# Kernel tuning notes

Measured on AMD Instinct MI355X. Metric: run time of the kernel, lower is better.

Reference implementation:

```python
import jax, jax.numpy as jnp
import numpy as np


def setup_inputs() -> dict:
    key = jax.random.key(0)
    ks = jax.random.split(key, 9)
    B, T, S, D = 4, 256, 256, 512
    scale = 1.0 / np.sqrt(D)
    inp = {
        "output": jax.random.normal(ks[0], (B, T, D), dtype=jnp.float32),
        "context": jax.random.normal(ks[1], (B, S, D), dtype=jnp.float32),
        "mask": jax.random.randint(ks[2], (B, S), 0, 2, dtype=jnp.int32),
        # learned params (nn.Linear stores y = x @ W.T + b; we store W.T directly)
        "Wq": jax.random.normal(ks[3], (D, D), dtype=jnp.float32) * scale,
        "bq": jax.random.normal(ks[4], (D,), dtype=jnp.float32) * scale,
        "Wc": jax.random.normal(ks[5], (D, D), dtype=jnp.float32) * scale,
        "v": jax.random.normal(ks[6], (D,), dtype=jnp.float32) * scale,
        "Wout": jax.random.normal(ks[7], (2 * D, D), dtype=jnp.float32) * scale,
        "bout": jax.random.normal(ks[8], (D,), dtype=jnp.float32) * scale,
    }
    return inp


def reference(output, context, mask, Wq, bq, Wc, v, Wout, bout):
    # output: (B, T, D) decoder states; context: (B, S, D) encoder states
    wq = jnp.einsum("btd,de->bte", output, Wq) + bq          # (B, T, D)
    uh = jnp.einsum("bsd,de->bse", context, Wc)               # (B, S, D)
    # additive score: v . tanh(wq + uh), broadcast over (T, S)
    wquh = jnp.tanh(wq[:, :, None, :] + uh[:, None, :, :])    # (B, T, S, D)
    score = jnp.einsum("btsd,d->bts", wquh, v)                # (B, T, S)
    # masked softmax exactly as the torch code: max over ALL positions,
    # then zero out masked entries (mask==1 means masked) and renormalize.
    max_by_row = jnp.max(score, axis=-1, keepdims=True)
    keep = (1.0 - mask.astype(score.dtype))[:, None, :]       # (B, 1, S)
    attn = jnp.exp(score - max_by_row) * keep
    attn = attn / jnp.sum(attn, axis=-1, keepdims=True)       # (B, T, S)
    mix = jnp.einsum("bts,bsd->btd", attn, context)           # (B, T, D)
    combined = jnp.concatenate([mix, output], axis=-1)        # (B, T, 2D)
    out = jnp.einsum("btf,fd->btd", combined, Wout) + bout    # (B, T, D)
    return out, attn
```

## Files before the change

### kernel.cpp

```cpp
#include <hip/hip_runtime.h>
#include <hip/hip_bf16.h>

#define B_ 4
#define T_ 256
#define S_ 256
#define D_ 512
#define TB 2

typedef __bf16 bf16x8 __attribute__((ext_vector_type(8)));
typedef float  floatx4 __attribute__((ext_vector_type(4)));
typedef float  floatx2 __attribute__((ext_vector_type(2)));

#define C2F 2.885390081777926f

static __device__ __forceinline__ unsigned short f2bf(float x) {
    __hip_bfloat16 h = __float2bfloat16(x);
    return *reinterpret_cast<unsigned short*>(&h);
}
static __device__ __forceinline__ float asf(unsigned int u) {
    float f; __builtin_memcpy(&f, &u, 4); return f;
}
static __device__ __forceinline__ float clamp_pos(float x) {
    return fminf(fmaxf(x, 1e-15f), 1e15f);
}


__global__ __launch_bounds__(256) void prep(
    const float* __restrict__ output, const float* __restrict__ context,
    const float* __restrict__ Wq, const float* __restrict__ Wc,
    const float* __restrict__ Wout,
    unsigned short* __restrict__ out_f, unsigned short* __restrict__ ctx_f,
    unsigned short* __restrict__ Wq_f, unsigned short* __restrict__ Wc_f,
    unsigned short* __restrict__ WoT_f, unsigned short* __restrict__ WoB_f)
{
    const int tid = threadIdx.x;
    const int z = blockIdx.z;

    if (z >= 4) {
        const float* src = (z == 4) ? output : context;
        unsigned short* dst = (z == 4) ? out_f : ctx_f;
        const int bid  = blockIdx.y * 16 + blockIdx.x;
        const int tile = bid * 4 + (tid >> 6);
        const int lane = tid & 63;
        const int mblk = tile >> 4, kblk = tile & 15;
        const float* s = src + (size_t)(mblk * 16 + (lane & 15)) * 512
                             + kblk * 32 + (lane >> 4) * 8;
        float4 a = *(const float4*)s;
        float4 b = *(const float4*)(s + 4);
        uint4 pk;
        pk.x = (unsigned)f2bf(a.x) | ((unsigned)f2bf(a.y) << 16);
        pk.y = (unsigned)f2bf(a.z) | ((unsigned)f2bf(a.w) << 16);
        pk.z = (unsigned)f2bf(b.x) | ((unsigned)f2bf(b.y) << 16);
        pk.w = (unsigned)f2bf(b.z) | ((unsigned)f2bf(b.w) << 16);
        *(uint4*)(dst + (size_t)tile * 512 + lane * 8) = pk;
        return;
    }

    const float* W; unsigned short* WF; int krow0;
    if      (z == 0) { W = Wq;   WF = Wq_f;  krow0 = 0;   }
    else if (z == 1) { W = Wc;   WF = Wc_f;  krow0 = 0;   }
    else if (z == 2) { W = Wout; WF = WoT_f; krow0 = 0;   }
    else             { W = Wout; WF = WoB_f; krow0 = 512; }

    const int n0 = blockIdx.x * 32;
    const int k0 = blockIdx.y * 32;

    __shared__ float tile[32][33];
    const int c = tid & 31, r = tid >> 5;
    #pragma unroll
    for (int i = 0; i < 4; ++i)
        tile[r + 8 * i][c] = W[(size_t)(krow0 + k0 + r + 8 * i) * 512 + n0 + c];
    __syncthreads();
    #pragma unroll
    for (int i = 0; i < 4; ++i) {
        const int n = n0 + r + 8 * i;
        const int k = k0 + c;
        const int tl = (n >> 4) * 16 + (k >> 5);
        const int ln = (n & 15) | (((k >> 3) & 3) << 4);
        WF[((size_t)tl * 64 + ln) * 8 + (k & 7)] = f2bf(tile[c][r + 8 * i]);
    }
}

struct GArgs {
    const unsigned short* Af;
    const unsigned short* Bf;
    const float* aux;
    void* C;
    int mode;
};

__global__ __launch_bounds__(256) void gemm2(GArgs g0, GArgs g1, GArgs g2, GArgs g3)
{
    const int z = blockIdx.z;
    GArgs g = (z == 0) ? g0 : (z == 1) ? g1 : (z == 2) ? g2 : g3;

    const int tid  = threadIdx.x;
    const int wave = tid >> 6, lane = tid & 63;
    const int l15  = lane & 15, quad = lane >> 4;
    const int mblk = blockIdx.y * 4 + wave;
    const int nb0  = blockIdx.x * 4;

    const unsigned short* Ap = g.Af + ((size_t)mblk * 16 * 64 + lane) * 8;
    const unsigned short* Bp = g.Bf + ((size_t)nb0 * 16 * 64 + lane) * 8;

    floatx4 acc[4];
    #pragma unroll
    for (int i = 0; i < 4; ++i) acc[i] = (floatx4){0.f, 0.f, 0.f, 0.f};

    #pragma unroll 4
    for (int k = 0; k < 16; ++k) {
        bf16x8 a  = *(const bf16x8*)(Ap + k * 512);
        #pragma unroll
        for (int ni = 0; ni < 4; ++ni) {
            bf16x8 b = *(const bf16x8*)(Bp + (size_t)ni * 16 * 512 + k * 512);
            acc[ni] = __builtin_amdgcn_mfma_f32_16x16x32_bf16(a, b, acc[ni], 0, 0, 0);
        }
    }

    #pragma unroll
    for (int ni = 0; ni < 4; ++ni) {
        const int col = (nb0 + ni) * 16 + l15;
        const int rbase = mblk * 16 + quad * 4;
        if (g.mode == 1) {
            float* Cf = (float*)g.C;
            float bv = g.aux[col];
            #pragma unroll
            for (int r = 0; r < 4; ++r) {
                float hh = __builtin_amdgcn_exp2f(C2F * (acc[ni][r] + bv));
                Cf[(size_t)(rbase + r) * 512 + col] = clamp_pos(hh);
            }
        } else if (g.mode == 3) {
            unsigned short* Cb = (unsigned short*)g.C;
            float rv = __builtin_amdgcn_rcpf(g.aux[col]);
            rv = fminf(fmaxf(rv, -1e30f), 1e30f);
            #pragma unroll
            for (int r = 0; r < 4; ++r) {
                int row = rbase + r, bb = row >> 8, ss = row & 255;
                float ww = __builtin_amdgcn_exp2f(C2F * acc[ni][r]) * rv;
                ww = fminf(fmaxf(ww, -1e20f), 1e20f);
                Cb[((size_t)(bb * 64 + (col >> 3)) * 256 + ss) * 8 + (col & 7)]
                    = f2bf(ww);
            }
        } else if (g.mode == 5) {
            unsigned short* Cb = (unsigned short*)g.C;
            #pragma unroll
            for (int r = 0; r < 4; ++r)
                Cb[(size_t)(rbase + r) * 512 + col] = f2bf(acc[ni][r]);
        } else {
            float* Cf = (float*)g.C;
            float bv = g.aux[col];
            #pragma unroll
            for (int r = 0; r < 4; ++r)
                Cf[(size_t)(rbase + r) * 512 + col] = acc[ni][r] + bv;
        }
    }
}

__global__ __launch_bounds__(512, 4) void attn_fused(
    const float* __restrict__ Hb,
    const unsigned short* __restrict__ Wb,
    const unsigned short* __restrict__ CWb,
    const float* __restrict__ OB,
    const int*   __restrict__ mask,
    const float* __restrict__ v,
    float* __restrict__ attn_out,
    float* __restrict__ out)
{
    const int bid = blockIdx.x;
    const int bg  = (bid & 7) * (B_ * T_ / TB / 8) + (bid >> 3);
    const int b   = bg / (T_ / TB);
    const int t0  = (bg % (T_ / TB)) * TB;
    const int tid = threadIdx.x;
    const int s   = tid & 255;
    const int h   = tid >> 8;

    __shared__ float  w_s[TB][D_];
    __shared__ float  v_s[D_];
    __shared__ float2 part[2][256];
    __shared__ float2 wred[4];
    __shared__ float  a_s[TB][256];
    __shared__ float  mixp[4][TB][D_];

    w_s[0][tid] = Hb[(size_t)(b * T_ + t0 + 0) * D_ + tid];
    w_s[1][tid] = Hb[(size_t)(b * T_ + t0 + 1) * D_ + tid];
    {
        float iv = __builtin_amdgcn_rcpf(v[tid]);
        v_s[tid] = fminf(fmaxf(iv, -1e30f), 1e30f);
    }
    __syncthreads();

    float acc0 = 0.f, acc1 = 0.f;
    const uint4* wb4 = (const uint4*)(Wb + ((size_t)(b * 64 + h * 32) * 256 + s) * 8);

    #pragma unroll 4
    for (int dd = 0; dd < 32; ++dd) {
        uint4 ww = wb4[(size_t)dd * 256];
        floatx2 W01 = {asf(ww.x << 16), asf(ww.x & 0xffff0000u)};
        floatx2 W23 = {asf(ww.y << 16), asf(ww.y & 0xffff0000u)};
        floatx2 W45 = {asf(ww.z << 16), asf(ww.z & 0xffff0000u)};
        floatx2 W67 = {asf(ww.w << 16), asf(ww.w & 0xffff0000u)};

        const int dbase = (h * 32 + dd) * 8;
        float4 iva = *(const float4*)&v_s[dbase];
        float4 ivb = *(const float4*)&v_s[dbase + 4];
        float4 h0a = *(const float4*)&w_s[0][dbase];
        float4 h0b = *(const float4*)&w_s[0][dbase + 4];
        float4 h1a = *(const float4*)&w_s[1][dbase];
        float4 h1b = *(const float4*)&w_s[1][dbase + 4];

        #define PAIR(Wp, Hx, Hy, Ix, Iy, A)                                     \
        {                                                                       \
            floatx2 hh = {Hx, Hy};                                              \
            floatx2 ii = {Ix, Iy};                                              \
            floatx2 x = __builtin_elementwise_fma(hh, Wp, ii);                  \
            A = fmaf(x.x + x.y, __builtin_amdgcn_rcpf(x.x * x.y), A);           \
        }
        PAIR(W01, h0a.x, h0a.y, iva.x, iva.y, acc0)
        PAIR(W01, h1a.x, h1a.y, iva.x, iva.y, acc1)
        PAIR(W23, h0a.z, h0a.w, iva.z, iva.w, acc0)
        PAIR(W23, h1a.z, h1a.w, iva.z, iva.w, acc1)
        PAIR(W45, h0b.x, h0b.y, ivb.x, ivb.y, acc0)
        PAIR(W45, h1b.x, h1b.y, ivb.x, ivb.y, acc1)
        PAIR(W67, h0b.z, h0b.w, ivb.z, ivb.w, acc0)
        PAIR(W67, h1b.z, h1b.w, ivb.z, ivb.w, acc1)
        #undef PAIR
    }
    part[h][s] = make_float2(acc0, acc1);
    __syncthreads();

    float p0 = 0.f, p1 = 0.f;
    if (tid < 256) {
        float A0 = part[0][tid].x + part[1][tid].x;
        float A1 = part[0][tid].y + part[1][tid].y;
        float keep = 1.0f - (float)mask[b * S_ + tid];
        p0 = __builtin_amdgcn_exp2f(-C2F * A0) * keep;
        p1 = __builtin_amdgcn_exp2f(-C2F * A1) * keep;
        float s0 = p0, s1 = p1;
        #pragma unroll
        for (int off = 1; off < 64; off <<= 1) {
            s0 += __shfl_xor(s0, off);
            s1 += __shfl_xor(s1, off);
        }
        if ((tid & 63) == 0) wred[tid >> 6] = make_float2(s0, s1);
    }
    __syncthreads();

    if (tid < 256) {
        float den0 = wred[0].x + wred[1].x + wred[2].x + wred[3].x;
        float den1 = wred[0].y + wred[1].y + wred[2].y + wred[3].y;
        float a0 = p0 * __builtin_amdgcn_rcpf(den0);
        float a1 = p1 * __builtin_amdgcn_rcpf(den1);
        attn_out[(size_t)(b * T_ + t0 + 0) * S_ + tid] = a0;
        attn_out[(size_t)(b * T_ + t0 + 1) * S_ + tid] = a1;
        a_s[0][tid] = a0;
        a_s[1][tid] = a1;
    }
    __syncthreads();

    const int dq = tid & 127, sq = tid >> 7;
    const int sh = sq * 64;
    const unsigned short* cw = CWb + ((size_t)(b * S_) + sh) * D_ + 4 * dq;
    float m[TB][4] = {};
    #pragma unroll 8
    for (int s2 = 0; s2 < 64; ++s2) {
        uint2 cc = *(const uint2*)(cw + (size_t)s2 * D_);
        float c0 = asf(cc.x << 16), c1 = asf(cc.x & 0xffff0000u);
        float c2 = asf(cc.y << 16), c3 = asf(cc.y & 0xffff0000u);
        #pragma unroll
        for (int t = 0; t < TB; ++t) {
            float a = a_s[t][sh + s2];
            m[t][0] = fmaf(a, c0, m[t][0]);
            m[t][1] = fmaf(a, c1, m[t][1]);
            m[t][2] = fmaf(a, c2, m[t][2]);
            m[t][3] = fmaf(a, c3, m[t][3]);
        }
    }
    #pragma unroll
    for (int t = 0; t < TB; ++t)
        *(float4*)&mixp[sq][t][4 * dq] = make_float4(m[t][0], m[t][1], m[t][2], m[t][3]);
    __syncthreads();

    {
        #pragma unroll
        for (int t = 0; t < TB; ++t) {
            const int d = tid;
            size_t idx = (size_t)(b * T_ + t0 + t) * D_ + d;
            out[idx] = mixp[0][t][d] + mixp[1][t][d] + mixp[2][t][d] + mixp[3][t][d]
                     + OB[idx];
        }
    }
}

extern "C" void kernel_launch(void* const* d_in, const int* in_sizes, int n_in,
                              void* d_out, int out_size, void* d_ws, size_t ws_size,
                              hipStream_t stream) {
    const float* output  = (const float*)d_in[0];
    const float* context = (const float*)d_in[1];
    const int*   mask    = (const int*)d_in[2];
    const float* Wq      = (const float*)d_in[3];
    const float* bq      = (const float*)d_in[4];
    const float* Wc      = (const float*)d_in[5];
    const float* v       = (const float*)d_in[6];
    const float* Wout    = (const float*)d_in[7];
    const float* bout    = (const float*)d_in[8];

    float* out  = (float*)d_out;
    float* attn = out + (size_t)B_ * T_ * D_;

    char* ws = (char*)d_ws;
    float* Hb             = (float*)ws;
    float* OB             = (float*)(ws + (2u << 20));
    unsigned short* Wb    = (unsigned short*)(ws + (4u << 20));
    unsigned short* out_f = (unsigned short*)(ws + (6u << 20));
    unsigned short* ctx_f = (unsigned short*)(ws + (7u << 20));
    unsigned short* Wq_f  = (unsigned short*)(ws + (8u << 20));
    unsigned short* Wc_f  = (unsigned short*)(ws + (8u << 20) + (512u << 10));
    unsigned short* WoT_f = (unsigned short*)(ws + (9u << 20));
    unsigned short* WoB_f = (unsigned short*)(ws + (9u << 20) + (512u << 10));
    unsigned short* CWb   = (unsigned short*)(ws + (10u << 20));

    dim3 blk(256);

    prep<<<dim3(16, 16, 6), blk, 0, stream>>>(
        output, context, Wq, Wc, Wout, out_f, ctx_f, Wq_f, Wc_f, WoT_f, WoB_f);

    GArgs gwq = { out_f, Wq_f,  bq,   Hb,  1 };
    GArgs guh = { ctx_f, Wc_f,  v,    Wb,  3 };
    GArgs gob = { out_f, WoB_f, bout, OB,  4 };
    GArgs gcw = { ctx_f, WoT_f, NULL, CWb, 5 };
    gemm2<<<dim3(8, 16, 4), blk, 0, stream>>>(gwq, guh, gob, gcw);

    attn_fused<<<dim3(B_ * T_ / TB), dim3(512), 0, stream>>>(
        Hb, Wb, CWb, OB, mask, v, attn, out);
}
```

Baseline: 112.2 us.

## Narrow GEMM N-tile, store output bias term in bf16, prefetch Wb in attention loop

Result: faster. 108.7 us (-3.2%).

```diff
diff --git a/kernel.cpp b/kernel.cpp
--- a/kernel.cpp
+++ b/kernel.cpp
@@ -98,27 +98,27 @@
     const int wave = tid >> 6, lane = tid & 63;
     const int l15  = lane & 15, quad = lane >> 4;
     const int mblk = blockIdx.y * 4 + wave;
-    const int nb0  = blockIdx.x * 4;
-
-    const unsigned short* Ap = g.Af + ((size_t)mblk * 16 * 64 + lane) * 8;
-    const unsigned short* Bp = g.Bf + ((size_t)nb0 * 16 * 64 + lane) * 8;
-
-    floatx4 acc[4];
-    #pragma unroll
-    for (int i = 0; i < 4; ++i) acc[i] = (floatx4){0.f, 0.f, 0.f, 0.f};
+    const int nb0  = blockIdx.x * 2;
+
+    const unsigned short* Ap  = g.Af + ((size_t)mblk * 16 * 64 + lane) * 8;
+    const unsigned short* Bp0 = g.Bf + ((size_t)nb0 * 16 * 64 + lane) * 8;
+    const unsigned short* Bp1 = Bp0 + (size_t)16 * 64 * 8;
+
+    floatx4 acc[2];
+    acc[0] = (floatx4){0.f, 0.f, 0.f, 0.f};
+    acc[1] = (floatx4){0.f, 0.f, 0.f, 0.f};
 
     #pragma unroll 4
     for (int k = 0; k < 16; ++k) {
-        bf16x8 a  = *(const bf16x8*)(Ap + k * 512);
-        #pragma unroll
-        for (int ni = 0; ni < 4; ++ni) {
-            bf16x8 b = *(const bf16x8*)(Bp + (size_t)ni * 16 * 512 + k * 512);
-            acc[ni] = __builtin_amdgcn_mfma_f32_16x16x32_bf16(a, b, acc[ni], 0, 0, 0);
-        }
-    }
-
-    #pragma unroll
-    for (int ni = 0; ni < 4; ++ni) {
+        bf16x8 a  = *(const bf16x8*)(Ap  + k * 512);
+        bf16x8 b0 = *(const bf16x8*)(Bp0 + k * 512);
+        bf16x8 b1 = *(const bf16x8*)(Bp1 + k * 512);
+        acc[0] = __builtin_amdgcn_mfma_f32_16x16x32_bf16(a, b0, acc[0], 0, 0, 0);
+        acc[1] = __builtin_amdgcn_mfma_f32_16x16x32_bf16(a, b1, acc[1], 0, 0, 0);
+    }
+
+    #pragma unroll
+    for (int ni = 0; ni < 2; ++ni) {
         const int col = (nb0 + ni) * 16 + l15;
         const int rbase = mblk * 16 + quad * 4;
         if (g.mode == 1) {
@@ -147,11 +147,11 @@
             for (int r = 0; r < 4; ++r)
                 Cb[(size_t)(rbase + r) * 512 + col] = f2bf(acc[ni][r]);
         } else {
-            float* Cf = (float*)g.C;
+            unsigned short* Cb = (unsigned short*)g.C;
             float bv = g.aux[col];
             #pragma unroll
             for (int r = 0; r < 4; ++r)
-                Cf[(size_t)(rbase + r) * 512 + col] = acc[ni][r] + bv;
+                Cb[(size_t)(rbase + r) * 512 + col] = f2bf(acc[ni][r] + bv);
         }
     }
 }
@@ -160,7 +160,7 @@
     const float* __restrict__ Hb,
     const unsigned short* __restrict__ Wb,
     const unsigned short* __restrict__ CWb,
-    const float* __restrict__ OB,
+    const unsigned short* __restrict__ OBb,
     const int*   __restrict__ mask,
     const float* __restrict__ v,
     float* __restrict__ attn_out,
@@ -192,38 +192,54 @@
     float acc0 = 0.f, acc1 = 0.f;
     const uint4* wb4 = (const uint4*)(Wb + ((size_t)(b * 64 + h * 32) * 256 + s) * 8);
 
-    #pragma unroll 4
-    for (int dd = 0; dd < 32; ++dd) {
-        uint4 ww = wb4[(size_t)dd * 256];
-        floatx2 W01 = {asf(ww.x << 16), asf(ww.x & 0xffff0000u)};
-        floatx2 W23 = {asf(ww.y << 16), asf(ww.y & 0xffff0000u)};
-        floatx2 W45 = {asf(ww.z << 16), asf(ww.z & 0xffff0000u)};
-        floatx2 W67 = {asf(ww.w << 16), asf(ww.w & 0xffff0000u)};
-
-        const int dbase = (h * 32 + dd) * 8;
-        float4 iva = *(const float4*)&v_s[dbase];
-        float4 ivb = *(const float4*)&v_s[dbase + 4];
-        float4 h0a = *(const float4*)&w_s[0][dbase];
-        float4 h0b = *(const float4*)&w_s[0][dbase + 4];
-        float4 h1a = *(const float4*)&w_s[1][dbase];
-        float4 h1b = *(const float4*)&w_s[1][dbase + 4];
-
-        #define PAIR(Wp, Hx, Hy, Ix, Iy, A)                                     \
-        {                                                                       \
-            floatx2 hh = {Hx, Hy};                                              \
-            floatx2 ii = {Ix, Iy};                                              \
-            floatx2 x = __builtin_elementwise_fma(hh, Wp, ii);                  \
-            A = fmaf(x.x + x.y, __builtin_amdgcn_rcpf(x.x * x.y), A);           \
-        }
-        PAIR(W01, h0a.x, h0a.y, iva.x, iva.y, acc0)
-        PAIR(W01, h1a.x, h1a.y, iva.x, iva.y, acc1)
-        PAIR(W23, h0a.z, h0a.w, iva.z, iva.w, acc0)
-        PAIR(W23, h1a.z, h1a.w, iva.z, iva.w, acc1)
-        PAIR(W45, h0b.x, h0b.y, ivb.x, ivb.y, acc0)
-        PAIR(W45, h1b.x, h1b.y, ivb.x, ivb.y, acc1)
-        PAIR(W67, h0b.z, h0b.w, ivb.z, ivb.w, acc0)
-        PAIR(W67, h1b.z, h1b.w, ivb.z, ivb.w, acc1)
-        #undef PAIR
+    uint4 buf0 = wb4[0 * 256];
+    uint4 buf1 = wb4[1 * 256];
+    uint4 buf2 = wb4[2 * 256];
+    uint4 buf3 = wb4[3 * 256];
+
+    #pragma unroll
+    for (int dd0 = 0; dd0 < 32; dd0 += 4) {
+        uint4 c0 = buf0, c1 = buf1, c2 = buf2, c3 = buf3;
+        if (dd0 + 4 < 32) {
+            buf0 = wb4[(size_t)(dd0 + 4) * 256];
+            buf1 = wb4[(size_t)(dd0 + 5) * 256];
+            buf2 = wb4[(size_t)(dd0 + 6) * 256];
+            buf3 = wb4[(size_t)(dd0 + 7) * 256];
+        }
+        #pragma unroll
+        for (int i = 0; i < 4; ++i) {
+            const uint4 ww = (i == 0) ? c0 : (i == 1) ? c1 : (i == 2) ? c2 : c3;
+            const int dd = dd0 + i;
+            floatx2 W01 = {asf(ww.x << 16), asf(ww.x & 0xffff0000u)};
+            floatx2 W23 = {asf(ww.y << 16), asf(ww.y & 0xffff0000u)};
+            floatx2 W45 = {asf(ww.z << 16), asf(ww.z & 0xffff0000u)};
+            floatx2 W67 = {asf(ww.w << 16), asf(ww.w & 0xffff0000u)};
+
+            const int dbase = (h * 32 + dd) * 8;
+            float4 iva = *(const float4*)&v_s[dbase];
+            float4 ivb = *(const float4*)&v_s[dbase + 4];
+            float4 h0a = *(const float4*)&w_s[0][dbase];
+            float4 h0b = *(const float4*)&w_s[0][dbase + 4];
+            float4 h1a = *(const float4*)&w_s[1][dbase];
+            float4 h1b = *(const float4*)&w_s[1][dbase + 4];
+
+            #define PAIR(Wp, Hx, Hy, Ix, Iy, A_)                                \
+            {                                                                   \
+                floatx2 hh = {Hx, Hy};                                          \
+                floatx2 ii = {Ix, Iy};                                          \
+                floatx2 x = __builtin_elementwise_fma(hh, Wp, ii);              \
+                A_ = fmaf(x.x + x.y, __builtin_amdgcn_rcpf(x.x * x.y), A_);     \
+            }
+            PAIR(W01, h0a.x, h0a.y, iva.x, iva.y, acc0)
+            PAIR(W01, h1a.x, h1a.y, iva.x, iva.y, acc1)
+            PAIR(W23, h0a.z, h0a.w, iva.z, iva.w, acc0)
+            PAIR(W23, h1a.z, h1a.w, iva.z, iva.w, acc1)
+            PAIR(W45, h0b.x, h0b.y, ivb.x, ivb.y, acc0)
+            PAIR(W45, h1b.x, h1b.y, ivb.x, ivb.y, acc1)
+            PAIR(W67, h0b.z, h0b.w, ivb.z, ivb.w, acc0)
+            PAIR(W67, h1b.z, h1b.w, ivb.z, ivb.w, acc1)
+            #undef PAIR
+        }
     }
     part[h][s] = make_float2(acc0, acc1);
     __syncthreads();
@@ -285,8 +301,9 @@
         for (int t = 0; t < TB; ++t) {
             const int d = tid;
             size_t idx = (size_t)(b * T_ + t0 + t) * D_ + d;
+            float ob = asf((unsigned)OBb[idx] << 16);
             out[idx] = mixp[0][t][d] + mixp[1][t][d] + mixp[2][t][d] + mixp[3][t][d]
-                     + OB[idx];
+                     + ob;
         }
     }
 }
@@ -309,7 +326,7 @@
 
     char* ws = (char*)d_ws;
     float* Hb             = (float*)ws;
-    float* OB             = (float*)(ws + (2u << 20));
+    unsigned short* OBb   = (unsigned short*)(ws + (2u << 20));
     unsigned short* Wb    = (unsigned short*)(ws + (4u << 20));
     unsigned short* out_f = (unsigned short*)(ws + (6u << 20));
     unsigned short* ctx_f = (unsigned short*)(ws + (7u << 20));
@@ -326,10 +343,10 @@
 
     GArgs gwq = { out_f, Wq_f,  bq,   Hb,  1 };
     GArgs guh = { ctx_f, Wc_f,  v,    Wb,  3 };
-    GArgs gob = { out_f, WoB_f, bout, OB,  4 };
+    GArgs gob = { out_f, WoB_f, bout, OBb, 4 };
     GArgs gcw = { ctx_f, WoT_f, NULL, CWb, 5 };
-    gemm2<<<dim3(8, 16, 4), blk, 0, stream>>>(gwq, guh, gob, gcw);
+    gemm2<<<dim3(16, 16, 4), blk, 0, stream>>>(gwq, guh, gob, gcw);
 
     attn_fused<<<dim3(B_ * T_ / TB), dim3(512), 0, stream>>>(
-        Hb, Wb, CWb, OB, mask, v, attn, out);
-}
+        Hb, Wb, CWb, OBb, mask, v, attn, out);
+}
```
